# Optimization experiments

Measured on AMD Instinct MI355X. Metric: run time of the kernel, lower is better.

## Reference

```python
import jax, jax.numpy as jnp
from jax import lax
import numpy as np

B, H, W, C = 4, 64, 64, 128
L = H * W
DI = 2 * C   # mamba d_inner (expand=2)
NS = 16      # d_state
R = C // 16  # dt_rank
K = 4        # d_conv
S = 4        # scan branches: fwd, bwd, extra1, extra2


def setup_inputs():
    key = jax.random.key(0)
    ks = jax.random.split(key, 20)
    g = lambda i, shape, s=0.02: jax.random.normal(ks[i], shape, jnp.float32) * s
    return {
        "I1": jax.random.normal(ks[0], (B, L, C), jnp.float32),
        "fusion_resi": jax.random.normal(ks[1], (B, L, C), jnp.float32),
        "I2": jax.random.normal(ks[2], (B, L, C), jnp.float32),
        "fusion": jax.random.normal(ks[3], (B, L, C), jnp.float32),
        "ln1_w": jnp.ones((C,)), "ln1_b": jnp.zeros((C,)),
        "ln2_w": jnp.ones((C,)), "ln2_b": jnp.zeros((C,)),
        "ln3_w": jnp.ones((C,)), "ln3_b": jnp.zeros((C,)),
        "sp_w": g(4, (1, 2, 5, 5), 0.1),
        "ca_w1": g(5, (C // 4, C), 0.05),
        "ca_w2": g(6, (C, C // 4), 0.05),
        "dw_w": g(7, (C, 1, 3, 3), 0.1),
        "dw_b": jnp.zeros((C,)),
        "in_proj_w": g(8, (2 * DI, C)),
        "in_proj1_w": g(9, (DI, C)),
        "in_proj2_w": g(10, (DI, C)),
        "conv_w": g(11, (S, DI, K), 0.1),
        "conv_b": jnp.zeros((S, DI)),
        "xproj_w": g(12, (S, R + 2 * NS, DI)),
        "dt_w": g(13, (S, DI, R), 0.1),
        "dt_b": jnp.full((S, DI), -4.6, jnp.float32),  # softplus -> dt ~ 0.01
        "A_log": jnp.broadcast_to(jnp.log(jnp.arange(1, NS + 1, dtype=jnp.float32)), (S, DI, NS)) * 1.0,
        "Dskip": jnp.ones((S, DI)),
        "out_w": g(14, (C, DI)),
        "test_h": H, "test_w": W,
    }


def ln(x, w, b):
    mu = x.mean(-1, keepdims=True)
    xc = x - mu
    v = (xc * xc).mean(-1, keepdims=True)
    return xc / jnp.sqrt(v + 1e-5) * w + b


def sp_att(x, w, h, wd):
    # x: (B, N, C) -> (B, N, 1) spatial attention map
    Bb = x.shape[0]
    m = jnp.concatenate([x.mean(2, keepdims=True), x.max(2, keepdims=True)], 2)
    m = m.transpose(0, 2, 1).reshape(Bb, 2, h, wd)
    o = lax.conv_general_dilated(m, w, (1, 1), [(2, 2), (2, 2)],
                                 dimension_numbers=("NCHW", "OIHW", "NCHW"))
    return jax.nn.sigmoid(o).reshape(Bb, 1, -1).transpose(0, 2, 1)


def mamba_m3(xf, e1, e2, in_proj_w, in_proj1_w, in_proj2_w, conv_w, conv_b,
             xproj_w, dt_w, dt_b, A_log, Dskip, out_w):
    Bb, Ll, _ = xf.shape
    xz = xf @ in_proj_w.T                       # (B,L,2DI)
    x, z = xz[..., :DI], xz[..., DI:]
    # 4 branches: forward, backward (flipped), extra_emb1, extra_emb2
    u = jnp.stack([x, x[:, ::-1], e1 @ in_proj1_w.T, e2 @ in_proj2_w.T], 0)  # (S,B,L,DI)

    def causal_dwconv(xb, w, b):                # xb (B,L,DI)
        xp = jnp.pad(xb.transpose(0, 2, 1), ((0, 0), (0, 0), (K - 1, 0)))
        o = lax.conv_general_dilated(xp, w[:, None, :], (1,), "VALID",
                                     feature_group_count=DI,
                                     dimension_numbers=("NCH", "OIH", "NCH"))
        return (o + b[None, :, None]).transpose(0, 2, 1)

    uc = jax.nn.silu(jax.vmap(causal_dwconv)(u, conv_w, conv_b))        # (S,B,L,DI)
    proj = jnp.einsum("sbld,spd->sblp", uc, xproj_w)
    dt = jax.nn.softplus(jnp.einsum("sblr,sdr->sbld", proj[..., :R], dt_w)
                         + dt_b[:, None, None, :])                      # (S,B,L,DI)
    Bm, Cm = proj[..., R:R + NS], proj[..., R + NS:]                    # (S,B,L,NS)
    A = -jnp.exp(A_log)                                                 # (S,DI,NS)

    def step(h, inp):
        dt_t, B_t, C_t, u_t = inp                                       # (S,B,DI),(S,B,NS),(S,B,NS),(S,B,DI)
        dA = jnp.exp(dt_t[..., None] * A[:, None])                      # (S,B,DI,NS)
        h = h * dA + (dt_t * u_t)[..., None] * B_t[:, :, None, :]
        return h, jnp.einsum("sbdn,sbn->sbd", h, C_t)

    xs = tuple(t.transpose(2, 0, 1, 3) for t in (dt, Bm, Cm, uc))
    h0 = jnp.zeros((S, Bb, DI, NS), xf.dtype)
    _, ys = lax.scan(step, h0, xs)                                      # (L,S,B,DI)
    y = ys.transpose(1, 2, 0, 3) + uc * Dskip[:, None, None, :]         # (S,B,L,DI)
    y_tot = y[0] + y[1][:, ::-1] + y[2] + y[3]
    return (y_tot * jax.nn.silu(z)) @ out_w.T


def reference(I1, fusion_resi, I2, fusion, ln1_w, ln1_b, ln2_w, ln2_b, ln3_w,
              ln3_b, sp_w, ca_w1, ca_w2, dw_w, dw_b, in_proj_w, in_proj1_w,
              in_proj2_w, conv_w, conv_b, xproj_w, dt_w, dt_b, A_log, Dskip,
              out_w, test_h, test_w):
    fusion_resi = fusion + fusion_resi
    fusion = ln(fusion_resi, ln1_w, ln1_b)
    I2 = ln(I2 * sp_att(I2, sp_w, test_h, test_w), ln2_w, ln2_b)
    I1 = ln(I1 * sp_att(I1, sp_w, test_h, test_w), ln3_w, ln3_b)
    # note: original applies norm1/norm2/norm3 a second time here (faithful)
    gf = mamba_m3(ln(fusion, ln1_w, ln1_b), ln(I2, ln2_w, ln2_b),
                  ln(I1, ln3_w, ln3_b), in_proj_w, in_proj1_w, in_proj2_w,
                  conv_w, conv_b, xproj_w, dt_w, dt_b, A_log, Dskip, out_w)
    Bb, _, Cc = gf.shape
    f4 = gf.transpose(0, 2, 1).reshape(Bb, Cc, test_h, test_w)
    # ChannelAttention1 (already returns x*sig) then extra *fusion per source
    fc = lambda v: jnp.maximum(v @ ca_w1.T, 0.0) @ ca_w2.T
    sig = jax.nn.sigmoid(fc(f4.mean((2, 3))) + fc(f4.max((2, 3))))[:, :, None, None]
    f4 = (f4 * sig) * f4
    dw = lax.conv_general_dilated(f4, dw_w, (1, 1), [(1, 1), (1, 1)],
                                  feature_group_count=Cc,
                                  dimension_numbers=("NCHW", "OIHW", "NCHW"))
    dw = dw + dw_b[None, :, None, None]
    out = (dw + f4).reshape(Bb, Cc, -1).transpose(0, 2, 1)
    return out, fusion_resi
```

## Files before the change

kernel.cpp:

```cpp
#include <hip/hip_runtime.h>

#define DEVI __device__ __forceinline__

static constexpr int BB=4, CC=128, LLn=4096, DI=256, NS=16, RR=8, SS=4;
static constexpr int PP = RR + 2*NS;
static constexpr int CT = 64, NCH = LLn/CT;
static constexpr size_t BLC  = (size_t)BB*LLn*CC;
static constexpr size_t BLD  = (size_t)BB*LLn*DI;
static constexpr size_t SBLD = (size_t)SS*BLD;
static constexpr size_t SBLP = (size_t)SS*BB*LLn*PP;

static constexpr int OW_LN1W=0, OW_LN1B=128, OW_LN2W=256, OW_LN2B=384, OW_LN3W=512, OW_LN3B=640,
 OW_SPW=768, OW_CAW1=820, OW_CAW2=4916, OW_DWW=9012, OW_DWB=10164, OW_IPW=10292,
 OW_IP1W=75828, OW_IP2W=108596, OW_CVW=141364, OW_CVB=145460, OW_XPW=146484,
 OW_DTW=187444, OW_DTB=195636, OW_ALOG=196660, OW_DSK=213044, OW_OUTW=214068;
static constexpr int NW_RAW = 246836;
static constexpr int NW_END = 246848;

__constant__ int c_woff[22] = {OW_LN1W,OW_LN1B,OW_LN2W,OW_LN2B,OW_LN3W,OW_LN3B,OW_SPW,OW_CAW1,
 OW_CAW2,OW_DWW,OW_DWB,OW_IPW,OW_IP1W,OW_IP2W,OW_CVW,OW_CVB,OW_XPW,OW_DTW,OW_DTB,OW_ALOG,
 OW_DSK,OW_OUTW};
__constant__ int c_wsz[22]  = {128,128,128,128,128,128,50,4096,4096,1152,128,65536,32768,32768,
 4096,1024,40960,8192,1024,16384,1024,32768};

static constexpr size_t O_XF   = NW_END;
static constexpr size_t O_E1   = O_XF + BLC;
static constexpr size_t O_E2   = O_E1 + BLC;
static constexpr size_t O_Z    = O_E2 + BLC;
static constexpr size_t O_U    = O_Z + BLD;
static constexpr size_t O_UC   = O_U + SBLD;
static constexpr size_t O_PROJ = O_UC + SBLD;
static constexpr size_t O_SDT  = O_PROJ + SBLP;
static constexpr size_t O_H    = O_SDT + (size_t)SS*BB*NCH*DI;
static constexpr size_t O_M    = O_H + (size_t)SS*BB*NCH*DI*NS;
static constexpr size_t O_S    = O_M + 2*(size_t)BB*2*LLn;
static constexpr size_t O_GF   = O_S + 2*(size_t)BB*LLn;
static constexpr size_t O_PART = O_GF + BLC;
static constexpr size_t O_SIG  = O_PART + 2*(size_t)BB*32*CC;
static constexpr size_t WS_END = O_SIG + (size_t)BB*CC;

typedef __attribute__((ext_vector_type(8))) short short8v;
typedef __attribute__((ext_vector_type(4))) float f32x4;

DEVI float bfu2f(unsigned short s){ union{unsigned u; float f;} c; c.u = ((unsigned)s)<<16; return c.f; }
DEVI unsigned short f2bfu(float f){ union{float f; unsigned u;} c; c.f=f;
  unsigned r = c.u + 0x7FFFu + ((c.u>>16)&1u); return (unsigned short)(r>>16); }
DEVI float4 bf4(uint2 v){ return make_float4(bfu2f((unsigned short)(v.x&0xFFFFu)), bfu2f((unsigned short)(v.x>>16)),
                                             bfu2f((unsigned short)(v.y&0xFFFFu)), bfu2f((unsigned short)(v.y>>16))); }
DEVI bool bfmode(const void* ln1w){ return *(const unsigned*)ln1w == 0x3F803F80u; }
DEVI float2 ldin2(const void* p, int i, bool isbf){
  if(isbf){ unsigned v = *(const unsigned*)((const unsigned short*)p + i);
    return make_float2(bfu2f((unsigned short)(v & 0xFFFFu)), bfu2f((unsigned short)(v >> 16))); }
  const float* f = (const float*)p + i; return make_float2(f[0], f[1]);
}
DEVI float wsum(float v){
#pragma unroll
  for(int o=32;o;o>>=1) v += __shfl_xor(v,o,64);
  return v; }
DEVI float wmaxr(float v){
#pragma unroll
  for(int o=32;o;o>>=1) v = fmaxf(v, __shfl_xor(v,o,64));
  return v; }
DEVI float sigf(float x){ return 1.f/(1.f+__expf(-x)); }
DEVI float2 ln_wave(float2 x, const float* Wf, int ow, int ob, int lane){
  float mu = wsum(x.x + x.y) * (1.f/(float)CC);
  float dx = x.x - mu, dy = x.y - mu;
  float var = wsum(dx*dx + dy*dy) * (1.f/(float)CC);
  float rs = rsqrtf(var + 1e-5f);
  int c = 2*lane;
  return make_float2(dx*rs*Wf[ow+c] + Wf[ob+c], dy*rs*Wf[ow+c+1] + Wf[ob+c+1]);
}

struct Srcs { const void* p[22]; };

__global__ void k_xwpad(unsigned* __restrict__ xw32){
  int i = blockIdx.x*256 + threadIdx.x;
  xw32[i] = 0u;
}

__global__ void k_wcvt(Srcs s, float* __restrict__ ws,
                       unsigned short* __restrict__ wip, unsigned short* __restrict__ wob,
                       unsigned short* __restrict__ xw){
  bool isbf = bfmode(s.p[0]);
  int idx = blockIdx.x*256 + threadIdx.x;
  if(idx >= NW_RAW) return;
  int t = 0;
  while(t < 21 && idx >= c_woff[t+1]) t++;
  int j = idx - c_woff[t];
  if(j >= c_wsz[t]) return;
  float v = isbf ? bfu2f(((const unsigned short*)s.p[t])[j]) : ((const float*)s.p[t])[j];
  ws[idx] = v;
  if(t==11)      wip[j]         = f2bfu(v);
  else if(t==12) wip[65536+j]   = f2bfu(v);
  else if(t==13) wip[98304+j]   = f2bfu(v);
  else if(t==21) wob[j]         = f2bfu(v);
  else if(t==16){
    int sid = j / 10240, rem = j % 10240;
    xw[((size_t)sid*64 + rem/256)*256 + (rem%256)] = f2bfu(v);
  }
}

__global__ void k_fuse(const void* fus, const void* fres, const void* ln1raw,
                       float* __restrict__ ws, float* __restrict__ outf,
                       unsigned short* __restrict__ xbf){
  bool isbf = bfmode(ln1raw);
  int lane = threadIdx.x & 63, wv = threadIdx.x >> 6;
  int row = blockIdx.x*4 + wv;
  int base = row*CC;
  float2 a = ldin2(fus, base+2*lane, isbf);
  float2 b = ldin2(fres, base+2*lane, isbf);
  float2 fr = make_float2(a.x+b.x, a.y+b.y);
  *(float2*)(outf + BLC + base + 2*lane) = fr;
  float2 y = ln_wave(fr, ws, OW_LN1W, OW_LN1B, lane);
  y = ln_wave(y, ws, OW_LN1W, OW_LN1B, lane);
  unsigned pk = (unsigned)f2bfu(y.x) | ((unsigned)f2bfu(y.y)<<16);
  *(unsigned*)&xbf[base + 2*lane] = pk;
}

__global__ void k_meanmax(const void* I1, const void* I2, const void* ln1raw, float* __restrict__ ws){
  bool isbf = bfmode(ln1raw);
  int lane = threadIdx.x & 63, wv = threadIdx.x >> 6;
  int g = blockIdx.x*4 + wv;
  int ten = g & 1, row = g >> 1;
  const void* src = ten ? I2 : I1;
  float2 x = ldin2(src, row*CC + 2*lane, isbf);
  float sm = wsum(x.x + x.y) * (1.f/(float)CC);
  float mx = wmaxr(fmaxf(x.x, x.y));
  if(lane == 0){
    int b = row >> 12, l = row & 4095;
    float* mt = ws + O_M + (size_t)ten*(BB*2*LLn);
    mt[(size_t)b*2*LLn + l] = sm;
    mt[(size_t)b*2*LLn + LLn + l] = mx;
  }
}

__global__ void k_spconv(float* __restrict__ ws){
  int idx = blockIdx.x*256 + threadIdx.x;
  int ten = idx >> 14, b = (idx>>12)&3, l = idx & 4095;
  int h = l >> 6, w = l & 63;
  const float* mt = ws + O_M + (size_t)ten*(BB*2*LLn) + (size_t)b*2*LLn;
  float acc = 0.f;
  for(int ci=0; ci<2; ci++)
    for(int kh=0; kh<5; kh++){
      int hh = h + kh - 2; if((unsigned)hh >= 64u) continue;
      for(int kw=0; kw<5; kw++){
        int wn = w + kw - 2; if((unsigned)wn >= 64u) continue;
        acc += mt[(size_t)ci*LLn + hh*64 + wn] * ws[OW_SPW + ci*25 + kh*5 + kw];
      }
    }
  ws[O_S + (size_t)ten*(BB*LLn) + (size_t)b*LLn + l] = sigf(acc);
}

__global__ void k_escale(const void* I1, const void* I2, const void* ln1raw,
                         float* __restrict__ ws, unsigned short* __restrict__ xbf){
  bool isbf = bfmode(ln1raw);
  int lane = threadIdx.x & 63, wv = threadIdx.x >> 6;
  int g = blockIdx.x*4 + wv;
  int ten = g & 1, row = g >> 1;
  const void* src = ten ? I1 : I2;
  float sc = ws[O_S + (ten ? 0 : (size_t)BB*LLn) + row];
  float2 x = ldin2(src, row*CC + 2*lane, isbf);
  x.x *= sc; x.y *= sc;
  int ow = ten ? OW_LN3W : OW_LN2W, ob = ten ? OW_LN3B : OW_LN2B;
  float2 y = ln_wave(x, ws, ow, ob, lane);
  y = ln_wave(y, ws, ow, ob, lane);
  unsigned short* eb = xbf + (ten ? 2*BLC : BLC);
  unsigned pk = (unsigned)f2bfu(y.x) | ((unsigned)f2bfu(y.y)<<16);
  *(unsigned*)&eb[row*CC + 2*lane] = pk;
}

__global__ __launch_bounds__(256) void k_gemm_bf(const unsigned short* __restrict__ Abf,
    const unsigned short* __restrict__ Wbf, float* __restrict__ out,
    int Kd, int N, int mode, unsigned short* __restrict__ ub16, float* __restrict__ z){
  __shared__ unsigned short As[64*64];
  __shared__ unsigned short Bs[64*64];
  const int tid = threadIdx.x, lane = tid & 63, w = tid >> 6;
  const int n0 = blockIdx.x*64, m0 = blockIdx.y*64;
  const int g = lane >> 4, rlo = lane & 15;
  if(mode == 2) Wbf += (size_t)(m0 >> 14) * (64*256);
  f32x4 acc[4];
#pragma unroll
  for(int i=0;i<4;i++) acc[i] = (f32x4){0.f,0.f,0.f,0.f};
  const int nk = Kd >> 6;
  for(int kt=0; kt<nk; kt++){
#pragma unroll
    for(int it=0; it<2; it++){
      int idx = it*256 + tid, r = idx>>3, c = idx&7;
      uint4 av = *(const uint4*)&Abf[(size_t)(m0+r)*Kd + kt*64 + c*8];
      uint4 bv = *(const uint4*)&Wbf[(size_t)(n0+r)*Kd + kt*64 + c*8];
      int sw = (c*16) ^ ((r&7)<<4);
      *(uint4*)((char*)As + r*128 + sw) = av;
      *(uint4*)((char*)Bs + r*128 + sw) = bv;
    }
    __syncthreads();
#pragma unroll
    for(int ks=0; ks<2; ks++){
      int kb = ks*64 + g*16;
      int brow = w*16 + rlo;
      short8v bf = *(short8v*)((char*)Bs + brow*128 + (kb ^ ((rlo&7)<<4)));
#pragma unroll
      for(int rt=0; rt<4; rt++){
        int arow = rt*16 + rlo;
        short8v af = *(short8v*)((char*)As + arow*128 + (kb ^ ((rlo&7)<<4)));
        acc[rt] = __builtin_amdgcn_mfma_f32_16x16x32_bf16(af, bf, acc[rt], 0, 0, 0);
      }
    }
    __syncthreads();
  }
#pragma unroll
  for(int rt=0; rt<4; rt++){
#pragma unroll
    for(int j=0; j<4; j++){
      int m = m0 + rt*16 + g*4 + j;
      int n = n0 + w*16 + rlo;
      float val = acc[rt][j];
      if(mode == 1){
        int b = m >> 12, l = m & (LLn-1);
        if(n < DI) ub16[((size_t)b*LLn + l)*DI + n] = f2bfu(val);
        else       z[((size_t)b*LLn + l)*DI + (n-DI)] = val;
      } else if(mode == 3){
        ub16[(size_t)m*N + n] = f2bfu(val);
      } else {
        if(n < N) out[(size_t)m*N + n] = val;
      }
    }
  }
}

__global__ void k_conv(const float* __restrict__ ws, const unsigned short* __restrict__ ubf,
                       unsigned short* __restrict__ ucbf){
  int t = blockIdx.x*256 + threadIdx.x;
  int dg = t & 63, lg = (t>>6) & 1023, sb = t >> 16, s = sb >> 2, b = sb & 3;
  int d0 = dg*4, l0 = lg*4;
  float wv[16];
  const float* wp = ws + OW_CVW + ((size_t)s*DI + d0)*4;
#pragma unroll
  for(int q=0;q<16;q++) wv[q] = wp[q];
  float4 cb = *(const float4*)&ws[OW_CVB + s*DI + d0];
  const bool rev = (s == 1);
  const unsigned short* ub = ubf + (rev ? (size_t)b*LLn : (size_t)sb*LLn)*DI;
  float4 w0, w1, w2;
  {
    int lm;
    lm = l0-3; w0 = (lm<0)?make_float4(0,0,0,0):bf4(*(const uint2*)&ub[(size_t)(rev?(LLn-1-lm):lm)*DI + d0]);
    lm = l0-2; w1 = (lm<0)?make_float4(0,0,0,0):bf4(*(const uint2*)&ub[(size_t)(rev?(LLn-1-lm):lm)*DI + d0]);
    lm = l0-1; w2 = (lm<0)?make_float4(0,0,0,0):bf4(*(const uint2*)&ub[(size_t)(rev?(LLn-1-lm):lm)*DI + d0]);
  }
#pragma unroll
  for(int r=0;r<4;r++){
    int l = l0 + r;
    float4 w3 = bf4(*(const uint2*)&ub[(size_t)(rev?(LLn-1-l):l)*DI + d0]);
    float4 acc;
    acc.x = cb.x + wv[0]*w0.x + wv[1]*w1.x + wv[2]*w2.x + wv[3]*w3.x;
    acc.y = cb.y + wv[4]*w0.y + wv[5]*w1.y + wv[6]*w2.y + wv[7]*w3.y;
    acc.z = cb.z + wv[8]*w0.z + wv[9]*w1.z + wv[10]*w2.z + wv[11]*w3.z;
    acc.w = cb.w + wv[12]*w0.w + wv[13]*w1.w + wv[14]*w2.w + wv[15]*w3.w;
    acc.x *= sigf(acc.x); acc.y *= sigf(acc.y); acc.z *= sigf(acc.z); acc.w *= sigf(acc.w);
    ushort4 o4; o4.x=f2bfu(acc.x); o4.y=f2bfu(acc.y); o4.z=f2bfu(acc.z); o4.w=f2bfu(acc.w);
    *(ushort4*)&ucbf[((size_t)sb*LLn + l)*DI + d0] = o4;
    w0 = w1; w1 = w2; w2 = w3;
  }
}

template<bool PH3>
__global__ __launch_bounds__(256) void k_scan(float* __restrict__ ws,
                                              const unsigned short* __restrict__ ucbf){
  __shared__ float pl[CT*PP];
  int ch = blockIdx.x & (NCH-1), sb = blockIdx.x >> 6, s = sb >> 2;
  int d = threadIdx.x;
  size_t prow = ((size_t)sb*LLn + (size_t)ch*CT)*PP;
#pragma unroll
  for(int i=0;i<10;i++){ int idx = i*256 + threadIdx.x; pl[idx] = ws[O_PROJ + prow + idx]; }
  __syncthreads();
  unsigned short* ybf = (unsigned short*)(ws + O_U);
  float4 dtw0 = *(const float4*)&ws[OW_DTW + ((size_t)s*DI + d)*RR];
  float4 dtw1 = *(const float4*)&ws[OW_DTW + ((size_t)s*DI + d)*RR + 4];
  float dtb = ws[OW_DTB + s*DI + d];
  float an2[NS]; bool fast = true;
#pragma unroll
  for(int n=0;n<NS;n++){
    float a = -__expf(ws[OW_ALOG + ((size_t)s*DI + d)*NS + n]);
    an2[n] = a * 1.44269504f;
    fast = fast && (fabsf(a + (float)(n+1)) < 1e-4f);
  }
  float4 h0,h1,h2,h3;
  size_t hb = (((size_t)sb*NCH + ch)*DI + d)*NS;
  float* H = ws + O_H;
  if(PH3){
    h0 = *(const float4*)&H[hb];    h1 = *(const float4*)&H[hb+4];
    h2 = *(const float4*)&H[hb+8];  h3 = *(const float4*)&H[hb+12];
  } else {
    h0=h1=h2=h3=make_float4(0.f,0.f,0.f,0.f);
  }
  float dsk = PH3 ? ws[OW_DSK + s*DI + d] : 0.f;
  float sdt = 0.f;
  size_t ub = ((size_t)sb*LLn + (size_t)ch*CT)*DI + d;
  if(fast){
    for(int ll=0; ll<CT; ll++){
      const float* pr = &pl[ll*PP];
      float4 p0 = *(const float4*)pr, p1 = *(const float4*)(pr+4);
      float x = dtb + p0.x*dtw0.x + p0.y*dtw0.y + p0.z*dtw0.z + p0.w*dtw0.w
                    + p1.x*dtw1.x + p1.y*dtw1.y + p1.z*dtw1.z + p1.w*dtw1.w;
      float dt = (x > 15.f) ? x : __logf(1.f + __expf(x));
      float ut = bfu2f(ucbf[ub + (size_t)ll*DI]);
      float du = dt*ut;
      float e = __expf(-dt);
      float e2 = e*e, e4 = e2*e2;
      float4 da = make_float4(e, e2, e2*e, e4);
      float4 B0 = *(const float4*)(pr+8),  B1 = *(const float4*)(pr+12),
             B2 = *(const float4*)(pr+16), B3 = *(const float4*)(pr+20);
      if(PH3){
        float4 C0 = *(const float4*)(pr+24), C1 = *(const float4*)(pr+28),
               C2 = *(const float4*)(pr+32), C3 = *(const float4*)(pr+36);
        float y;
        h0.x = fmaf(h0.x, da.x, du*B0.x); y  = h0.x*C0.x;
        h0.y = fmaf(h0.y, da.y, du*B0.y); y = fmaf(h0.y, C0.y, y);
        h0.z = fmaf(h0.z, da.z, du*B0.z); y = fmaf(h0.z, C0.z, y);
        h0.w = fmaf(h0.w, da.w, du*B0.w); y = fmaf(h0.w, C0.w, y);
        da.x *= e4; da.y *= e4; da.z *= e4; da.w *= e4;
        h1.x = fmaf(h1.x, da.x, du*B1.x); y = fmaf(h1.x, C1.x, y);
        h1.y = fmaf(h1.y, da.y, du*B1.y); y = fmaf(h1.y, C1.y, y);
        h1.z = fmaf(h1.z, da.z, du*B1.z); y = fmaf(h1.z, C1.z, y);
        h1.w = fmaf(h1.w, da.w, du*B1.w); y = fmaf(h1.w, C1.w, y);
        da.x *= e4; da.y *= e4; da.z *= e4; da.w *= e4;
        h2.x = fmaf(h2.x, da.x, du*B2.x); y = fmaf(h2.x, C2.x, y);
        h2.y = fmaf(h2.y, da.y, du*B2.y); y = fmaf(h2.y, C2.y, y);
        h2.z = fmaf(h2.z, da.z, du*B2.z); y = fmaf(h2.z, C2.z, y);
        h2.w = fmaf(h2.w, da.w, du*B2.w); y = fmaf(h2.w, C2.w, y);
        da.x *= e4; da.y *= e4; da.z *= e4; da.w *= e4;
        h3.x = fmaf(h3.x, da.x, du*B3.x); y = fmaf(h3.x, C3.x, y);
        h3.y = fmaf(h3.y, da.y, du*B3.y); y = fmaf(h3.y, C3.y, y);
        h3.z = fmaf(h3.z, da.z, du*B3.z); y = fmaf(h3.z, C3.z, y);
        h3.w = fmaf(h3.w, da.w, du*B3.w); y = fmaf(h3.w, C3.w, y);
        ybf[ub + (size_t)ll*DI] = f2bfu(y + ut*dsk);
      } else {
        h0.x = fmaf(h0.x, da.x, du*B0.x); h0.y = fmaf(h0.y, da.y, du*B0.y);
        h0.z = fmaf(h0.z, da.z, du*B0.z); h0.w = fmaf(h0.w, da.w, du*B0.w);
        da.x *= e4; da.y *= e4; da.z *= e4; da.w *= e4;
        h1.x = fmaf(h1.x, da.x, du*B1.x); h1.y = fmaf(h1.y, da.y, du*B1.y);
        h1.z = fmaf(h1.z, da.z, du*B1.z); h1.w = fmaf(h1.w, da.w, du*B1.w);
        da.x *= e4; da.y *= e4; da.z *= e4; da.w *= e4;
        h2.x = fmaf(h2.x, da.x, du*B2.x); h2.y = fmaf(h2.y, da.y, du*B2.y);
        h2.z = fmaf(h2.z, da.z, du*B2.z); h2.w = fmaf(h2.w, da.w, du*B2.w);
        da.x *= e4; da.y *= e4; da.z *= e4; da.w *= e4;
        h3.x = fmaf(h3.x, da.x, du*B3.x); h3.y = fmaf(h3.y, da.y, du*B3.y);
        h3.z = fmaf(h3.z, da.z, du*B3.z); h3.w = fmaf(h3.w, da.w, du*B3.w);
        sdt += dt;
      }
    }
  } else {
    float h[NS];
    h[0]=h0.x;h[1]=h0.y;h[2]=h0.z;h[3]=h0.w; h[4]=h1.x;h[5]=h1.y;h[6]=h1.z;h[7]=h1.w;
    h[8]=h2.x;h[9]=h2.y;h[10]=h2.z;h[11]=h2.w; h[12]=h3.x;h[13]=h3.y;h[14]=h3.z;h[15]=h3.w;
    for(int ll=0; ll<CT; ll++){
      const float* pr = &pl[ll*PP];
      float x = dtb;
      x += pr[0]*dtw0.x + pr[1]*dtw0.y + pr[2]*dtw0.z + pr[3]*dtw0.w;
      x += pr[4]*dtw1.x + pr[5]*dtw1.y + pr[6]*dtw1.z + pr[7]*dtw1.w;
      float dt = (x > 15.f) ? x : __logf(1.f + __expf(x));
      float ut = bfu2f(ucbf[ub + (size_t)ll*DI]);
      float du = dt*ut;
      if(PH3){
        float y = 0.f;
#pragma unroll
        for(int n=0;n<NS;n++){ float da = exp2f(an2[n]*dt); h[n] = h[n]*da + du*pr[RR+n]; y += h[n]*pr[RR+NS+n]; }
        ybf[ub + (size_t)ll*DI] = f2bfu(y + ut*dsk);
      } else {
#pragma unroll
        for(int n=0;n<NS;n++){ float da = exp2f(an2[n]*dt); h[n] = h[n]*da + du*pr[RR+n]; }
        sdt += dt;
      }
    }
    h0=make_float4(h[0],h[1],h[2],h[3]); h1=make_float4(h[4],h[5],h[6],h[7]);
    h2=make_float4(h[8],h[9],h[10],h[11]); h3=make_float4(h[12],h[13],h[14],h[15]);
  }
  if(!PH3){
    *(float4*)&H[hb]    = h0; *(float4*)&H[hb+4]  = h1;
    *(float4*)&H[hb+8]  = h2; *(float4*)&H[hb+12] = h3;
    ws[O_SDT + ((size_t)sb*NCH + ch)*DI + d] = sdt;
  }
}

__global__ void k_scan2(float* __restrict__ ws){
  int t = blockIdx.x*256 + threadIdx.x;
  int n = t & (NS-1), d = (t>>4) & (DI-1), sb = t >> 12, s = sb >> 2;
  float an2 = -__expf(ws[OW_ALOG + ((size_t)s*DI + d)*NS + n]) * 1.44269504f;
  float hin = 0.f;
  float* H = ws + O_H;
  for(int c=0;c<NCH;c++){
    size_t hi = (((size_t)sb*NCH + c)*DI + d)*NS + n;
    float he = H[hi];
    float sd = ws[O_SDT + ((size_t)sb*NCH + c)*DI + d];
    H[hi] = hin;
    hin = he + exp2f(an2*sd)*hin;
  }
}

__global__ void k_gate(float* __restrict__ ws, unsigned short* __restrict__ gbf){
  int t = blockIdx.x*256 + threadIdx.x;
  int d4 = t & 63, l = (t>>6)&4095, b = t>>18;
  int d0 = d4*4;
  const unsigned short* ybf = (const unsigned short*)(ws + O_U);
  size_t i0 = ((size_t)(0*BB+b)*LLn + l)*DI + d0;
  size_t i1 = ((size_t)(1*BB+b)*LLn + (LLn-1-l))*DI + d0;
  size_t i2 = ((size_t)(2*BB+b)*LLn + l)*DI + d0;
  size_t i3 = ((size_t)(3*BB+b)*LLn + l)*DI + d0;
  float4 a = bf4(*(const uint2*)&ybf[i0]);
  float4 bb4 = bf4(*(const uint2*)&ybf[i1]);
  float4 c = bf4(*(const uint2*)&ybf[i2]);
  float4 dd = bf4(*(const uint2*)&ybf[i3]);
  size_t zi = ((size_t)b*LLn + l)*DI + d0;
  float4 zv = *(const float4*)&ws[O_Z + zi];
  float4 g;
  g.x = (a.x+bb4.x+c.x+dd.x) * (zv.x*sigf(zv.x));
  g.y = (a.y+bb4.y+c.y+dd.y) * (zv.y*sigf(zv.y));
  g.z = (a.z+bb4.z+c.z+dd.z) * (zv.z*sigf(zv.z));
  g.w = (a.w+bb4.w+c.w+dd.w) * (zv.w*sigf(zv.w));
  uint2 pk;
  pk.x = (unsigned)f2bfu(g.x) | ((unsigned)f2bfu(g.y)<<16);
  pk.y = (unsigned)f2bfu(g.z) | ((unsigned)f2bfu(g.w)<<16);
  *(uint2*)&gbf[zi] = pk;
}

__global__ void k_redmm(float* __restrict__ ws){
  int b = blockIdx.x >> 5, seg = blockIdx.x & 31, c = threadIdx.x;
  const float* gf = ws + O_GF;
  float sm = 0.f, mx = -3e38f;
  size_t base = ((size_t)b*LLn + (size_t)seg*128)*CC + c;
  for(int i=0;i<128;i++){ float v = gf[base + (size_t)i*CC]; sm += v; mx = fmaxf(mx, v); }
  ws[O_PART + ((size_t)b*32 + seg)*CC + c] = sm;
  ws[O_PART + (size_t)BB*32*CC + ((size_t)b*32 + seg)*CC + c] = mx;
}

__global__ void k_catt(float* __restrict__ ws){
  __shared__ float vm[CC], vx[CC], hm[32], hx[32];
  int b = blockIdx.x, c = threadIdx.x;
  float sm = 0.f, mx = -3e38f;
  for(int seg=0;seg<32;seg++){
    sm += ws[O_PART + ((size_t)b*32+seg)*CC + c];
    mx = fmaxf(mx, ws[O_PART + (size_t)BB*32*CC + ((size_t)b*32+seg)*CC + c]);
  }
  vm[c] = sm * (1.f/(float)LLn); vx[c] = mx;
  __syncthreads();
  if(c < 32){
    float am = 0.f, ax = 0.f;
    for(int k=0;k<CC;k++){ float w1 = ws[OW_CAW1 + c*CC + k]; am += vm[k]*w1; ax += vx[k]*w1; }
    hm[c] = fmaxf(am, 0.f); hx[c] = fmaxf(ax, 0.f);
  }
  __syncthreads();
  float om = 0.f, ox = 0.f;
  for(int k=0;k<32;k++){ float w2 = ws[OW_CAW2 + c*32 + k]; om += hm[k]*w2; ox += hx[k]*w2; }
  ws[O_SIG + (size_t)b*CC + c] = sigf(om + ox);
}

__global__ void k_final(float* __restrict__ ws, float* __restrict__ outf){
  int t = blockIdx.x*256 + threadIdx.x;
  int c4 = t & 31, l = (t>>5)&4095, b = t>>17;
  int h = l>>6, w = l&63;
  const float* gf = ws + O_GF;
  float4 sg = *(const float4*)&ws[O_SIG + (size_t)b*CC + c4*4];
  size_t rb = ((size_t)b*LLn)*CC;
  float4 gc = *(const float4*)&gf[rb + (size_t)l*CC + c4*4];
  float4 fc = make_float4(gc.x*gc.x*sg.x, gc.y*gc.y*sg.y, gc.z*gc.z*sg.z, gc.w*gc.w*sg.w);
  float4 acc = *(const float4*)&ws[OW_DWB + c4*4];
  float wv[4][9];
#pragma unroll
  for(int j=0;j<4;j++)
#pragma unroll
    for(int q=0;q<9;q++) wv[j][q] = ws[OW_DWW + (c4*4+j)*9 + q];
#pragma unroll
  for(int kh=0;kh<3;kh++){
    int hh = h + kh - 1; if((unsigned)hh >= 64u) continue;
#pragma unroll
    for(int kw=0;kw<3;kw++){
      int wn = w + kw - 1; if((unsigned)wn >= 64u) continue;
      float4 g = *(const float4*)&gf[rb + (size_t)(hh*64+wn)*CC + c4*4];
      int q = kh*3+kw;
      acc.x += wv[0][q]*g.x*g.x*sg.x;
      acc.y += wv[1][q]*g.y*g.y*sg.y;
      acc.z += wv[2][q]*g.z*g.z*sg.z;
      acc.w += wv[3][q]*g.w*g.w*sg.w;
    }
  }
  float4 o = make_float4(acc.x+fc.x, acc.y+fc.y, acc.z+fc.z, acc.w+fc.w);
  size_t ob = ((size_t)b*LLn + l)*CC + c4*4;
  *(float4*)&outf[ob] = o;
}

extern "C" void kernel_launch(void* const* d_in, const int* in_sizes, int n_in,
                              void* d_out, int out_size, void* d_ws, size_t ws_size,
                              hipStream_t stream){
  (void)in_sizes; (void)n_in; (void)out_size;
  if(ws_size < WS_END*sizeof(float)) return;
  float* ws = (float*)d_ws;
  float* outf = (float*)d_out;
  const void* I1 = d_in[0]; const void* FRES = d_in[1];
  const void* I2 = d_in[2]; const void* FUS  = d_in[3];
  const void* LN1RAW = d_in[4];

  unsigned short* xbf   = (unsigned short*)(ws + O_H);
  unsigned short* gbf   = xbf;
  unsigned short* wipbf = (unsigned short*)(ws + O_GF);
  unsigned short* wobf  = (unsigned short*)(ws + O_PART);
  unsigned short* xwbf  = (unsigned short*)(ws + O_XF);
  unsigned short* ucbf  = (unsigned short*)(ws + O_UC);
  unsigned short* ubf   = (unsigned short*)(ws + O_U);

  Srcs sr;
  for(int i=0;i<22;i++) sr.p[i] = d_in[4+i];
  k_xwpad<<<128, 256, 0, stream>>>((unsigned*)xwbf);
  k_wcvt<<<(NW_RAW+255)/256, 256, 0, stream>>>(sr, ws, wipbf, wobf, xwbf);
  k_fuse<<<4096, 256, 0, stream>>>(FUS, FRES, LN1RAW, ws, outf, xbf);
  k_meanmax<<<8192, 256, 0, stream>>>(I1, I2, LN1RAW, ws);
  k_spconv<<<128, 256, 0, stream>>>(ws);
  k_escale<<<8192, 256, 0, stream>>>(I1, I2, LN1RAW, ws, xbf);
  k_gemm_bf<<<dim3(8,256), 256, 0, stream>>>(xbf,         wipbf,       nullptr,      128, 512, 1, ubf,        ws+O_Z);
  k_gemm_bf<<<dim3(4,256), 256, 0, stream>>>(xbf+BLC,     wipbf+65536, nullptr,      128, 256, 3, ubf+2*BLD,  nullptr);
  k_gemm_bf<<<dim3(4,256), 256, 0, stream>>>(xbf+2*BLC,   wipbf+98304, nullptr,      128, 256, 3, ubf+3*BLD,  nullptr);
  k_conv<<<4096, 256, 0, stream>>>(ws, ubf, ucbf);
  k_gemm_bf<<<dim3(1,1024), 256, 0, stream>>>(ucbf, xwbf, ws+O_PROJ, 256, 40, 2, nullptr, nullptr);
  k_scan<false><<<SS*BB*NCH, 256, 0, stream>>>(ws, ucbf);
  k_scan2<<<256, 256, 0, stream>>>(ws);
  k_scan<true><<<SS*BB*NCH, 256, 0, stream>>>(ws, ucbf);
  k_gate<<<4096, 256, 0, stream>>>(ws, gbf);
  k_gemm_bf<<<dim3(2,256), 256, 0, stream>>>(gbf, wobf, ws+O_GF, 256, 128, 0, nullptr, nullptr);
  k_redmm<<<128, 128, 0, stream>>>(ws);
  k_catt<<<4, 128, 0, stream>>>(ws);
  k_final<<<2048, 256, 0, stream>>>(ws, outf);
}
```

Measured before the change: 241.0 us.

## Halve scan chunk length and store chunk states and dt sums in bf16

```diff
diff --git a/kernel.cpp b/kernel.cpp
--- a/kernel.cpp
+++ b/kernel.cpp
@@ -4,7 +4,8 @@
 
 static constexpr int BB=4, CC=128, LLn=4096, DI=256, NS=16, RR=8, SS=4;
 static constexpr int PP = RR + 2*NS;
-static constexpr int CT = 64, NCH = LLn/CT;
+static constexpr int CT = 32, NCH = LLn/CT;
+static constexpr int NCHF = 64;
 static constexpr size_t BLC  = (size_t)BB*LLn*CC;
 static constexpr size_t BLD  = (size_t)BB*LLn*DI;
 static constexpr size_t SBLD = (size_t)SS*BLD;
@@ -31,8 +32,8 @@
 static constexpr size_t O_UC   = O_U + SBLD;
 static constexpr size_t O_PROJ = O_UC + SBLD;
 static constexpr size_t O_SDT  = O_PROJ + SBLP;
-static constexpr size_t O_H    = O_SDT + (size_t)SS*BB*NCH*DI;
-static constexpr size_t O_M    = O_H + (size_t)SS*BB*NCH*DI*NS;
+static constexpr size_t O_H    = O_SDT + (size_t)SS*BB*NCHF*DI;
+static constexpr size_t O_M    = O_H + (size_t)SS*BB*NCHF*DI*NS;
 static constexpr size_t O_S    = O_M + 2*(size_t)BB*2*LLn;
 static constexpr size_t O_GF   = O_S + 2*(size_t)BB*LLn;
 static constexpr size_t O_PART = O_GF + BLC;
@@ -47,6 +48,9 @@
   unsigned r = c.u + 0x7FFFu + ((c.u>>16)&1u); return (unsigned short)(r>>16); }
 DEVI float4 bf4(uint2 v){ return make_float4(bfu2f((unsigned short)(v.x&0xFFFFu)), bfu2f((unsigned short)(v.x>>16)),
                                              bfu2f((unsigned short)(v.y&0xFFFFu)), bfu2f((unsigned short)(v.y>>16))); }
+DEVI uint2 pk4(float4 v){ uint2 p;
+  p.x = (unsigned)f2bfu(v.x) | ((unsigned)f2bfu(v.y)<<16);
+  p.y = (unsigned)f2bfu(v.z) | ((unsigned)f2bfu(v.w)<<16); return p; }
 DEVI bool bfmode(const void* ln1w){ return *(const unsigned*)ln1w == 0x3F803F80u; }
 DEVI float2 ldin2(const void* p, int i, bool isbf){
   if(isbf){ unsigned v = *(const unsigned*)((const unsigned short*)p + i);
@@ -266,13 +270,15 @@
 __global__ __launch_bounds__(256) void k_scan(float* __restrict__ ws,
                                               const unsigned short* __restrict__ ucbf){
   __shared__ float pl[CT*PP];
-  int ch = blockIdx.x & (NCH-1), sb = blockIdx.x >> 6, s = sb >> 2;
+  int ch = blockIdx.x & (NCH-1), sb = blockIdx.x >> 7, s = sb >> 2;
   int d = threadIdx.x;
   size_t prow = ((size_t)sb*LLn + (size_t)ch*CT)*PP;
 #pragma unroll
-  for(int i=0;i<10;i++){ int idx = i*256 + threadIdx.x; pl[idx] = ws[O_PROJ + prow + idx]; }
+  for(int i=0;i<5;i++){ int idx = i*256 + threadIdx.x; pl[idx] = ws[O_PROJ + prow + idx]; }
   __syncthreads();
   unsigned short* ybf = (unsigned short*)(ws + O_U);
+  unsigned short* Hb  = (unsigned short*)(ws + O_H);
+  unsigned short* Sdb = (unsigned short*)(ws + O_SDT);
   float4 dtw0 = *(const float4*)&ws[OW_DTW + ((size_t)s*DI + d)*RR];
   float4 dtw1 = *(const float4*)&ws[OW_DTW + ((size_t)s*DI + d)*RR + 4];
   float dtb = ws[OW_DTB + s*DI + d];
@@ -285,10 +291,11 @@
   }
   float4 h0,h1,h2,h3;
   size_t hb = (((size_t)sb*NCH + ch)*DI + d)*NS;
-  float* H = ws + O_H;
   if(PH3){
-    h0 = *(const float4*)&H[hb];    h1 = *(const float4*)&H[hb+4];
-    h2 = *(const float4*)&H[hb+8];  h3 = *(const float4*)&H[hb+12];
+    uint4 ha = *(const uint4*)&Hb[hb];
+    uint4 hc = *(const uint4*)&Hb[hb+8];
+    h0 = bf4(make_uint2(ha.x,ha.y)); h1 = bf4(make_uint2(ha.z,ha.w));
+    h2 = bf4(make_uint2(hc.x,hc.y)); h3 = bf4(make_uint2(hc.z,hc.w));
   } else {
     h0=h1=h2=h3=make_float4(0.f,0.f,0.f,0.f);
   }
@@ -375,9 +382,10 @@
     h2=make_float4(h[8],h[9],h[10],h[11]); h3=make_float4(h[12],h[13],h[14],h[15]);
   }
   if(!PH3){
-    *(float4*)&H[hb]    = h0; *(float4*)&H[hb+4]  = h1;
-    *(float4*)&H[hb+8]  = h2; *(float4*)&H[hb+12] = h3;
-    ws[O_SDT + ((size_t)sb*NCH + ch)*DI + d] = sdt;
+    uint2 a = pk4(h0), b2 = pk4(h1), c = pk4(h2), dd = pk4(h3);
+    *(uint4*)&Hb[hb]   = make_uint4(a.x,a.y,b2.x,b2.y);
+    *(uint4*)&Hb[hb+8] = make_uint4(c.x,c.y,dd.x,dd.y);
+    Sdb[((size_t)sb*NCH + ch)*DI + d] = f2bfu(sdt);
   }
 }
 
@@ -386,12 +394,13 @@
   int n = t & (NS-1), d = (t>>4) & (DI-1), sb = t >> 12, s = sb >> 2;
   float an2 = -__expf(ws[OW_ALOG + ((size_t)s*DI + d)*NS + n]) * 1.44269504f;
   float hin = 0.f;
-  float* H = ws + O_H;
+  unsigned short* Hb  = (unsigned short*)(ws + O_H);
+  const unsigned short* Sdb = (const unsigned short*)(ws + O_SDT);
   for(int c=0;c<NCH;c++){
     size_t hi = (((size_t)sb*NCH + c)*DI + d)*NS + n;
-    float he = H[hi];
-    float sd = ws[O_SDT + ((size_t)sb*NCH + c)*DI + d];
-    H[hi] = hin;
+    float he = bfu2f(Hb[hi]);
+    float sd = bfu2f(Sdb[((size_t)sb*NCH + c)*DI + d]);
+    Hb[hi] = f2bfu(hin);
     hin = he + exp2f(an2*sd)*hin;
   }
 }
@@ -416,10 +425,7 @@
   g.y = (a.y+bb4.y+c.y+dd.y) * (zv.y*sigf(zv.y));
   g.z = (a.z+bb4.z+c.z+dd.z) * (zv.z*sigf(zv.z));
   g.w = (a.w+bb4.w+c.w+dd.w) * (zv.w*sigf(zv.w));
-  uint2 pk;
-  pk.x = (unsigned)f2bfu(g.x) | ((unsigned)f2bfu(g.y)<<16);
-  pk.y = (unsigned)f2bfu(g.z) | ((unsigned)f2bfu(g.w)<<16);
-  *(uint2*)&gbf[zi] = pk;
+  *(uint2*)&gbf[zi] = pk4(g);
 }
 
 __global__ void k_redmm(float* __restrict__ ws){
```

After: 250.2 us. 1.04x slower.
